# Performance work log

Hardware: AMD Instinct MI355X
Metric: run time of the kernel (lower is better)

## Reference

```python
import jax, jax.numpy as jnp
import numpy as np

N_NODES = 50000
N_EDGES = 800000
D_IN = 128
D_HID = 128
D_OUT = 128
EPS = 0.1  # GINConv eps


def setup_inputs() -> dict:
    key = jax.random.key(0)
    k = jax.random.split(key, 8)
    scale = 1.0 / np.sqrt(D_IN)
    return {
        "x": jax.random.normal(k[0], (N_NODES, D_IN), dtype=jnp.float32),
        "edge_index": jax.random.randint(k[1], (2, N_EDGES), 0, N_NODES, dtype=jnp.int64),
        "edge_weight": jax.random.uniform(k[2], (N_EDGES,), dtype=jnp.float32),
        "W1a": jax.random.normal(k[3], (D_IN, D_HID), dtype=jnp.float32) * scale,
        "W1b": jax.random.normal(k[4], (D_HID, D_HID), dtype=jnpp.float32) if False else jax.random.normal(k[4], (D_HID, D_HID), dtype=jnp.float32) * scale,
        "W2a": jax.random.normal(k[5], (D_HID, D_HID), dtype=jnp.float32) * scale,
        "W2b": jax.random.normal(k[6], (D_HID, D_OUT), dtype=jnp.float32) * scale,
    }


def _gin_conv(h, src, dst, ew, Wa, Wb, n_nodes):
    # edge-weighted neighbor sum: aggr[i] = sum_{(j->i)} w_ji * h[j]
    msg = ew[:, None] * h[src]                       # [E, d]
    aggr = jax.ops.segment_sum(msg, dst, num_segments=n_nodes)  # [N, d]
    z = (1.0 + EPS) * h + aggr                       # GIN update
    # 2-layer bias-free MLP: lin -> relu -> lin
    return jnp.maximum(z @ Wa, 0.0) @ Wb


def reference(x, edge_index, edge_weight, W1a, W1b, W2a, W2b):
    src, dst = edge_index[0], edge_index[1]
    n = x.shape[0]
    h = _gin_conv(x, src, dst, edge_weight, W1a, W1b, n)
    h = jnp.maximum(h, 0.0)  # relu between convs; dropout is identity in eval
    h = _gin_conv(h, src, dst, edge_weight, W2a, W2b, n)
    return h
```

## Files before the change

### kernel.cpp

```cpp
#include <hip/hip_runtime.h>
#include <hip/hip_fp16.h>

#define D 128
#define N_NODES 50000
#define EPSP1 1.1f

#define NPB 128
#define NBUCK 391
#define CAP 2560
#define P1E 4096
#define TS 136

typedef __attribute__((ext_vector_type(8))) short short8;
typedef __attribute__((ext_vector_type(4))) float f32x4;

__device__ __forceinline__ unsigned short f2bf(float f) {
    unsigned u = __float_as_uint(f);
    u += 0x7FFF + ((u >> 16) & 1);
    return (unsigned short)(u >> 16);
}
__device__ __forceinline__ float bf2f(unsigned short h) {
    return __uint_as_float(((unsigned)h) << 16);
}

__global__ __launch_bounds__(512, 4) void pass1_all(
    const int* __restrict__ src, const int* __restrict__ dst,
    const float* __restrict__ ew, int* __restrict__ gcnt,
    uint2* __restrict__ gstage, int ne, int nb1,
    const float* __restrict__ x, unsigned short* __restrict__ hb,
    int n4, int ncvt,
    const float* __restrict__ W1a, const float* __restrict__ W1b,
    const float* __restrict__ W2a, const float* __restrict__ W2b,
    unsigned short* __restrict__ wp)
{
    __shared__ int bcnt[NBUCK];
    __shared__ int goff[NBUCK];
    int tid = threadIdx.x;
    int bid = blockIdx.x;

    if (bid < nb1) {
        for (int i = tid; i < NBUCK; i += 512) bcnt[i] = 0;
        __syncthreads();
        int e0 = bid * P1E;
        int   rank[8];
        int   buck[8];
        uint2 pay[8];
#pragma unroll
        for (int j = 0; j < 8; ++j) {
            int e = e0 + j * 512 + tid;
            buck[j] = -1;
            if (e < ne) {
                int d_ = dst[e];
                int b  = d_ >> 7;
                int dl = d_ & 127;
                pay[j].x = (unsigned)(src[e] & 0xFFFF) | ((unsigned)dl << 16);
                pay[j].y = (unsigned)__half_as_ushort(__float2half_rn(ew[e]));
                rank[j]  = atomicAdd(&bcnt[b], 1);
                buck[j]  = b;
            }
        }
        __syncthreads();
        for (int i = tid; i < NBUCK; i += 512)
            if (bcnt[i] > 0) goff[i] = atomicAdd(&gcnt[i], bcnt[i]);
        __syncthreads();
#pragma unroll
        for (int j = 0; j < 8; ++j) {
            if (buck[j] >= 0) {
                int pos = goff[buck[j]] + rank[j];
                if (pos < CAP)
                    gstage[(size_t)buck[j] * CAP + pos] = pay[j];
            }
        }
    } else if (bid < nb1 + ncvt) {
        int base = (bid - nb1) * 4096;
#pragma unroll
        for (int it = 0; it < 8; ++it) {
            int i = base + it * 512 + tid;
            if (i < n4) {
                float4 v = ((const float4*)x)[i];
                ushort4 o;
                o.x = f2bf(v.x); o.y = f2bf(v.y); o.z = f2bf(v.z); o.w = f2bf(v.w);
                ((ushort4*)hb)[i] = o;
            }
        }
    } else {
        int e2 = (bid - nb1 - ncvt) * 512 + tid;
        if (e2 < 8192) {
            int mat = e2 >> 11;
            int e   = e2 & 2047;
            const float* W = (mat == 0) ? W1a : (mat == 1) ? W1b : (mat == 2) ? W2a : W2b;
            unsigned short* Wp = wp + (size_t)mat * 16384;
            int col = e & 127;
            int kq  = e >> 7;
            short8 v;
#pragma unroll
            for (int j = 0; j < 8; ++j)
                v[j] = (short)f2bf(W[(size_t)(kq * 8 + j) * 128 + col]);
            ((short8*)Wp)[e] = v;
        }
    }
}

__global__ __launch_bounds__(512) void csr_build(
    const uint2* __restrict__ gstage, const int* __restrict__ gcnt,
    unsigned* __restrict__ epay, int* __restrict__ off)
{
    __shared__ int hist[NPB];
    __shared__ int scn[NPB];
    __shared__ int loc[NPB];
    __shared__ int wtot[2];
    __shared__ int base_s;
    __shared__ unsigned csr[CAP];

    int b = blockIdx.x;
    int t = threadIdx.x;
    int cnt = min(gcnt[b], CAP);

    if (t < NPB) hist[t] = 0;
    __syncthreads();

    uint2 ent[CAP / 512];
#pragma unroll
    for (int it = 0; it < CAP / 512; ++it) {
        int i = it * 512 + t;
        if (i < cnt) {
            ent[it] = gstage[(size_t)b * CAP + i];
            atomicAdd(&hist[(ent[it].x >> 16) & 255], 1);
        }
    }
    __syncthreads();

    int w = t >> 6, l = t & 63;
    if (w < 2) {
        int v = hist[w * 64 + l];
#pragma unroll
        for (int dd = 1; dd < 64; dd <<= 1) {
            int u = __shfl_up(v, dd, 64);
            if (l >= dd) v += u;
        }
        scn[w * 64 + l] = v;
        if (l == 63) wtot[w] = v;
    } else if (w == 2) {
        int v = 0;
        for (int i = l; i < NBUCK; i += 64)
            if (i < b) v += min(gcnt[i], CAP);
#pragma unroll
        for (int dd = 32; dd > 0; dd >>= 1) v += __shfl_down(v, dd, 64);
        if (l == 0) base_s = v;
    }
    __syncthreads();

    if (t < NPB) {
        int pre = (t >= 64) ? wtot[0] : 0;
        int incl = scn[t] + pre;
        int excl = incl - hist[t];
        int node = (b << 7) + t;
        if (node <= N_NODES) off[node] = base_s + excl;
        loc[t] = excl;
    }
    __syncthreads();

#pragma unroll
    for (int it = 0; it < CAP / 512; ++it) {
        int i = it * 512 + t;
        if (i < cnt) {
            int dl = (ent[it].x >> 16) & 255;
            int p = atomicAdd(&loc[dl], 1);
            csr[p] = (ent[it].x & 0xFFFF) | (ent[it].y << 16);
        }
    }
    __syncthreads();

    for (int i = t; i < cnt; i += 512)
        epay[base_s + i] = csr[i];
}

template<int RELU2, int OUT_F32>
__global__ __launch_bounds__(512, 8) void conv_fused(
    const unsigned short* __restrict__ h, const int* __restrict__ off,
    const unsigned* __restrict__ epay,
    const unsigned short* __restrict__ WpA,
    const unsigned short* __restrict__ WpB,
    void* __restrict__ outv, int n)
{
    __shared__ unsigned short t1[32 * TS];
    __shared__ unsigned short t2[32 * TS];
    __shared__ int offs[33];

    int tid  = threadIdx.x;
    int wave = tid >> 6;
    int lane = tid & 63;
    int qtr  = lane >> 4;
    int sub  = lane & 15;
    int nb   = blockIdx.x * 32;

    if (tid < 33) offs[tid] = off[min(nb + tid, n)];
    __syncthreads();

    int row  = wave * 4 + qtr;
    int node = nb + row;
    int beg = offs[row];
    int end = offs[row + 1];

    float acc[8];
#pragma unroll
    for (int c = 0; c < 8; ++c) acc[c] = 0.f;

    int i = beg;
    for (; i + 4 <= end; i += 4) {
        unsigned p0 = epay[i];
        unsigned p1 = epay[i + 1];
        unsigned p2 = epay[i + 2];
        unsigned p3 = epay[i + 3];
        short8 v0 = ((const short8*)(h + (size_t)(p0 & 0xFFFF) * D))[sub];
        short8 v1 = ((const short8*)(h + (size_t)(p1 & 0xFFFF) * D))[sub];
        short8 v2 = ((const short8*)(h + (size_t)(p2 & 0xFFFF) * D))[sub];
        short8 v3 = ((const short8*)(h + (size_t)(p3 & 0xFFFF) * D))[sub];
        float w0 = __half2float(__ushort_as_half((unsigned short)(p0 >> 16)));
        float w1 = __half2float(__ushort_as_half((unsigned short)(p1 >> 16)));
        float w2 = __half2float(__ushort_as_half((unsigned short)(p2 >> 16)));
        float w3 = __half2float(__ushort_as_half((unsigned short)(p3 >> 16)));
#pragma unroll
        for (int c = 0; c < 8; ++c)
            acc[c] += w0 * bf2f((unsigned short)v0[c]) + w1 * bf2f((unsigned short)v1[c])
                    + w2 * bf2f((unsigned short)v2[c]) + w3 * bf2f((unsigned short)v3[c]);
    }
    for (; i < end; ++i) {
        unsigned p0 = epay[i];
        short8 v0 = ((const short8*)(h + (size_t)(p0 & 0xFFFF) * D))[sub];
        float w0 = __half2float(__ushort_as_half((unsigned short)(p0 >> 16)));
#pragma unroll
        for (int c = 0; c < 8; ++c)
            acc[c] += w0 * bf2f((unsigned short)v0[c]);
    }

    {
        const short8 zero8 = {0, 0, 0, 0, 0, 0, 0, 0};
        short8 o;
        if (node < n) {
            short8 xv = ((const short8*)(h + (size_t)node * D))[sub];
#pragma unroll
            for (int c = 0; c < 8; ++c)
                o[c] = (short)f2bf(acc[c] + EPSP1 * bf2f((unsigned short)xv[c]));
        } else {
            o = zero8;
        }
        *(short8*)&t1[row * TS + sub * 8] = o;
    }
    __syncthreads();

    int cf = wave;
    f32x4 acc2[2];
    acc2[0] = (f32x4){0.f, 0.f, 0.f, 0.f};
    acc2[1] = (f32x4){0.f, 0.f, 0.f, 0.f};

#pragma unroll
    for (int kk = 0; kk < 4; ++kk) {
        short8 a0 = *(const short8*)&t1[(sub)      * TS + kk * 32 + qtr * 8];
        short8 a1 = *(const short8*)&t1[(16 + sub) * TS + kk * 32 + qtr * 8];
        short8 b  = *(const short8*)(WpA + ((size_t)(kk * 4 + qtr) * 128 + cf * 16 + sub) * 8);
        acc2[0] = __builtin_amdgcn_mfma_f32_16x16x32_bf16(a0, b, acc2[0], 0, 0, 0);
        acc2[1] = __builtin_amdgcn_mfma_f32_16x16x32_bf16(a1, b, acc2[1], 0, 0, 0);
    }

#pragma unroll
    for (int s = 0; s < 2; ++s)
#pragma unroll
        for (int reg = 0; reg < 4; ++reg) {
            int r = s * 16 + qtr * 4 + reg;
            t2[r * TS + cf * 16 + sub] = f2bf(fmaxf(acc2[s][reg], 0.f));
        }
    __syncthreads();

    acc2[0] = (f32x4){0.f, 0.f, 0.f, 0.f};
    acc2[1] = (f32x4){0.f, 0.f, 0.f, 0.f};

#pragma unroll
    for (int kk = 0; kk < 4; ++kk) {
        short8 a0 = *(const short8*)&t2[(sub)      * TS + kk * 32 + qtr * 8];
        short8 a1 = *(const short8*)&t2[(16 + sub) * TS + kk * 32 + qtr * 8];
        short8 b  = *(const short8*)(WpB + ((size_t)(kk * 4 + qtr) * 128 + cf * 16 + sub) * 8);
        acc2[0] = __builtin_amdgcn_mfma_f32_16x16x32_bf16(a0, b, acc2[0], 0, 0, 0);
        acc2[1] = __builtin_amdgcn_mfma_f32_16x16x32_bf16(a1, b, acc2[1], 0, 0, 0);
    }

#pragma unroll
    for (int s = 0; s < 2; ++s)
#pragma unroll
        for (int reg = 0; reg < 4; ++reg) {
            int r = nb + s * 16 + qtr * 4 + reg;
            if (r < n) {
                float v = acc2[s][reg];
                if (RELU2) v = fmaxf(v, 0.f);
                int col = cf * 16 + sub;
                if (OUT_F32)
                    ((float*)outv)[(size_t)r * D + col] = v;
                else
                    ((unsigned short*)outv)[(size_t)r * D + col] = f2bf(v);
            }
        }
}

extern "C" void kernel_launch(void* const* d_in, const int* in_sizes, int n_in,
                              void* d_out, int out_size, void* d_ws, size_t ws_size,
                              hipStream_t stream) {
    const float* x   = (const float*)d_in[0];
    const int*   ei  = (const int*)d_in[1];
    const float* ew  = (const float*)d_in[2];
    const float* W1a = (const float*)d_in[3];
    const float* W1b = (const float*)d_in[4];
    const float* W2a = (const float*)d_in[5];
    const float* W2b = (const float*)d_in[6];
    float* out = (float*)d_out;

    int n_edges = in_sizes[2];
    const int* src = ei;
    const int* dst = ei + n_edges;

    size_t node_elems = (size_t)N_NODES * D;
    unsigned short* hb = (unsigned short*)d_ws;
    unsigned short* zb = hb + node_elems;
    unsigned short* wp = zb + node_elems;
    unsigned* epay = (unsigned*)(wp + 4 * 16384);
    uint2*  gstage = (uint2*)(epay + n_edges);
    int*    gcnt   = (int*)(gstage + (size_t)NBUCK * CAP);
    int*    off    = gcnt + NBUCK;

    int nb1   = (n_edges + P1E - 1) / P1E;
    int n4    = (int)(node_elems / 4);
    int ncvt  = (n4 + 4095) / 4096;
    int npack = 16;
    int cgrid = (N_NODES + 31) / 32;

    hipMemsetAsync(gcnt, 0, NBUCK * sizeof(int), stream);

    pass1_all<<<nb1 + ncvt + npack, 512, 0, stream>>>(
        src, dst, ew, gcnt, gstage, n_edges, nb1,
        x, hb, n4, ncvt, W1a, W1b, W2a, W2b, wp);

    csr_build<<<NBUCK, 512, 0, stream>>>(gstage, gcnt, epay, off);

    unsigned short* wp0 = wp;
    unsigned short* wp1 = wp + 16384;
    unsigned short* wp2 = wp + 2 * 16384;
    unsigned short* wp3 = wp + 3 * 16384;

    conv_fused<1, 0><<<cgrid, 512, 0, stream>>>(hb, off, epay, wp0, wp1, zb, N_NODES);

    conv_fused<0, 1><<<cgrid, 512, 0, stream>>>(zb, off, epay, wp2, wp3, out, N_NODES);
}
```

Measured before the change: 177.9 us.

## Merge all stages into one persistent kernel with software grid barriers

Replaces the four separate kernel launches (bucketing, CSR build, two GIN convolutions) with one persistent kernel of 512 blocks. The blocks loop over work units per stage and separate stages with an atomic-counter grid barrier, and shared memory is overlaid through a union. This removes the launch gaps and tail drain between kernels. In exchange, the conv stages lose occupancy (launch bounds of 4 waves instead of 8, and a fixed 512-block grid), and correctness depends on all 512 blocks being co-resident.

```diff
diff --git a/kernel.cpp b/kernel.cpp
--- a/kernel.cpp
+++ b/kernel.cpp
@@ -10,6 +10,7 @@
 #define CAP 2560
 #define P1E 4096
 #define TS 136
+#define PGRID 512
 
 typedef __attribute__((ext_vector_type(8))) short short8;
 typedef __attribute__((ext_vector_type(4))) float f32x4;
@@ -23,25 +24,48 @@
     return __uint_as_float(((unsigned)h) << 16);
 }
 
-__global__ __launch_bounds__(512, 4) void pass1_all(
+__device__ __forceinline__ void gsync(unsigned* bar) {
+    __syncthreads();
+    if (threadIdx.x == 0) {
+        __threadfence();
+        unsigned old = atomicAdd(bar, 1u);
+        unsigned tgt = (old / PGRID + 1u) * PGRID;
+        while (__hip_atomic_load(bar, __ATOMIC_RELAXED,
+                                 __HIP_MEMORY_SCOPE_AGENT) < tgt)
+            __builtin_amdgcn_s_sleep(2);
+        __threadfence();
+    }
+    __syncthreads();
+}
+
+struct SmemP1 { int bcnt[NBUCK]; int goff[NBUCK]; };
+struct SmemCsr {
+    int hist[NPB]; int scn[NPB]; int loc[NPB];
+    int wtot[2]; int base_s;
+    unsigned csr[CAP];
+};
+struct SmemConv {
+    unsigned short t1[32 * TS];
+    unsigned short t2[32 * TS];
+    int offs[33];
+};
+union SmemAll { SmemP1 p1; SmemCsr c; SmemConv v; };
+
+__device__ __forceinline__ void p1_unit(
+    int u, int nb1, int ncvt, SmemAll& sm,
     const int* __restrict__ src, const int* __restrict__ dst,
     const float* __restrict__ ew, int* __restrict__ gcnt,
-    uint2* __restrict__ gstage, int ne, int nb1,
-    const float* __restrict__ x, unsigned short* __restrict__ hb,
-    int n4, int ncvt,
+    uint2* __restrict__ gstage, int ne,
+    const float* __restrict__ x, unsigned short* __restrict__ hb, int n4,
     const float* __restrict__ W1a, const float* __restrict__ W1b,
     const float* __restrict__ W2a, const float* __restrict__ W2b,
     unsigned short* __restrict__ wp)
 {
-    __shared__ int bcnt[NBUCK];
-    __shared__ int goff[NBUCK];
     int tid = threadIdx.x;
-    int bid = blockIdx.x;
-
-    if (bid < nb1) {
-        for (int i = tid; i < NBUCK; i += 512) bcnt[i] = 0;
+    if (u < nb1) {
+        for (int i = tid; i < NBUCK; i += 512) sm.p1.bcnt[i] = 0;
         __syncthreads();
-        int e0 = bid * P1E;
+        int e0 = u * P1E;
         int   rank[8];
         int   buck[8];
         uint2 pay[8];
@@ -55,24 +79,25 @@
                 int dl = d_ & 127;
                 pay[j].x = (unsigned)(src[e] & 0xFFFF) | ((unsigned)dl << 16);
                 pay[j].y = (unsigned)__half_as_ushort(__float2half_rn(ew[e]));
-                rank[j]  = atomicAdd(&bcnt[b], 1);
+                rank[j]  = atomicAdd(&sm.p1.bcnt[b], 1);
                 buck[j]  = b;
             }
         }
         __syncthreads();
         for (int i = tid; i < NBUCK; i += 512)
-            if (bcnt[i] > 0) goff[i] = atomicAdd(&gcnt[i], bcnt[i]);
+            if (sm.p1.bcnt[i] > 0) sm.p1.goff[i] = atomicAdd(&gcnt[i], sm.p1.bcnt[i]);
         __syncthreads();
 #pragma unroll
         for (int j = 0; j < 8; ++j) {
             if (buck[j] >= 0) {
-                int pos = goff[buck[j]] + rank[j];
+                int pos = sm.p1.goff[buck[j]] + rank[j];
                 if (pos < CAP)
                     gstage[(size_t)buck[j] * CAP + pos] = pay[j];
             }
         }
-    } else if (bid < nb1 + ncvt) {
-        int base = (bid - nb1) * 4096;
+        __syncthreads();
+    } else if (u < nb1 + ncvt) {
+        int base = (u - nb1) * 4096;
 #pragma unroll
         for (int it = 0; it < 8; ++it) {
             int i = base + it * 512 + tid;
@@ -84,7 +109,7 @@
             }
         }
     } else {
-        int e2 = (bid - nb1 - ncvt) * 512 + tid;
+        int e2 = (u - nb1 - ncvt) * 512 + tid;
         if (e2 < 8192) {
             int mat = e2 >> 11;
             int e   = e2 & 2047;
@@ -101,22 +126,15 @@
     }
 }
 
-__global__ __launch_bounds__(512) void csr_build(
+__device__ __forceinline__ void csr_unit(
+    int b, SmemAll& sm,
     const uint2* __restrict__ gstage, const int* __restrict__ gcnt,
     unsigned* __restrict__ epay, int* __restrict__ off)
 {
-    __shared__ int hist[NPB];
-    __shared__ int scn[NPB];
-    __shared__ int loc[NPB];
-    __shared__ int wtot[2];
-    __shared__ int base_s;
-    __shared__ unsigned csr[CAP];
-
-    int b = blockIdx.x;
     int t = threadIdx.x;
     int cnt = min(gcnt[b], CAP);
 
-    if (t < NPB) hist[t] = 0;
+    if (t < NPB) sm.c.hist[t] = 0;
     __syncthreads();
 
     uint2 ent[CAP / 512];
@@ -125,38 +143,38 @@
         int i = it * 512 + t;
         if (i < cnt) {
             ent[it] = gstage[(size_t)b * CAP + i];
-            atomicAdd(&hist[(ent[it].x >> 16) & 255], 1);
+            atomicAdd(&sm.c.hist[(ent[it].x >> 16) & 255], 1);
         }
     }
     __syncthreads();
 
     int w = t >> 6, l = t & 63;
     if (w < 2) {
-        int v = hist[w * 64 + l];
+        int v = sm.c.hist[w * 64 + l];
 #pragma unroll
         for (int dd = 1; dd < 64; dd <<= 1) {
             int u = __shfl_up(v, dd, 64);
             if (l >= dd) v += u;
         }
-        scn[w * 64 + l] = v;
-        if (l == 63) wtot[w] = v;
+        sm.c.scn[w * 64 + l] = v;
+        if (l == 63) sm.c.wtot[w] = v;
     } else if (w == 2) {
         int v = 0;
         for (int i = l; i < NBUCK; i += 64)
             if (i < b) v += min(gcnt[i], CAP);
 #pragma unroll
         for (int dd = 32; dd > 0; dd >>= 1) v += __shfl_down(v, dd, 64);
-        if (l == 0) base_s = v;
+        if (l == 0) sm.c.base_s = v;
     }
     __syncthreads();
 
     if (t < NPB) {
-        int pre = (t >= 64) ? wtot[0] : 0;
-        int incl = scn[t] + pre;
-        int excl = incl - hist[t];
+        int pre = (t >= 64) ? sm.c.wtot[0] : 0;
+        int incl = sm.c.scn[t] + pre;
+        int excl = incl - sm.c.hist[t];
         int node = (b << 7) + t;
-        if (node <= N_NODES) off[node] = base_s + excl;
-        loc[t] = excl;
+        if (node <= N_NODES) off[node] = sm.c.base_s + excl;
+        sm.c.loc[t] = excl;
     }
     __syncthreads();
 
@@ -165,42 +183,41 @@
         int i = it * 512 + t;
         if (i < cnt) {
             int dl = (ent[it].x >> 16) & 255;
-            int p = atomicAdd(&loc[dl], 1);
-            csr[p] = (ent[it].x & 0xFFFF) | (ent[it].y << 16);
-        }
-    }
-    __syncthreads();
-
+            int p = atomicAdd(&sm.c.loc[dl], 1);
+            sm.c.csr[p] = (ent[it].x & 0xFFFF) | (ent[it].y << 16);
+        }
+    }
+    __syncthreads();
+
+    int base_s = sm.c.base_s;
     for (int i = t; i < cnt; i += 512)
-        epay[base_s + i] = csr[i];
+        epay[base_s + i] = sm.c.csr[i];
+    __syncthreads();
 }
 
 template<int RELU2, int OUT_F32>
-__global__ __launch_bounds__(512, 8) void conv_fused(
+__device__ __forceinline__ void conv_unit(
+    int u, SmemAll& sm,
     const unsigned short* __restrict__ h, const int* __restrict__ off,
     const unsigned* __restrict__ epay,
     const unsigned short* __restrict__ WpA,
     const unsigned short* __restrict__ WpB,
     void* __restrict__ outv, int n)
 {
-    __shared__ unsigned short t1[32 * TS];
-    __shared__ unsigned short t2[32 * TS];
-    __shared__ int offs[33];
-
     int tid  = threadIdx.x;
     int wave = tid >> 6;
     int lane = tid & 63;
     int qtr  = lane >> 4;
     int sub  = lane & 15;
-    int nb   = blockIdx.x * 32;
-
-    if (tid < 33) offs[tid] = off[min(nb + tid, n)];
+    int nb   = u * 32;
+
+    if (tid < 33) sm.v.offs[tid] = off[min(nb + tid, n)];
     __syncthreads();
 
     int row  = wave * 4 + qtr;
     int node = nb + row;
-    int beg = offs[row];
-    int end = offs[row + 1];
+    int beg = sm.v.offs[row];
+    int end = sm.v.offs[row + 1];
 
     float acc[8];
 #pragma unroll
@@ -245,7 +262,7 @@
         } else {
             o = zero8;
         }
-        *(short8*)&t1[row * TS + sub * 8] = o;
+        *(short8*)&sm.v.t1[row * TS + sub * 8] = o;
     }
     __syncthreads();
 
@@ -256,8 +273,8 @@
 
 #pragma unroll
     for (int kk = 0; kk < 4; ++kk) {
-        short8 a0 = *(const short8*)&t1[(sub)      * TS + kk * 32 + qtr * 8];
-        short8 a1 = *(const short8*)&t1[(16 + sub) * TS + kk * 32 + qtr * 8];
+        short8 a0 = *(const short8*)&sm.v.t1[(sub)      * TS + kk * 32 + qtr * 8];
+        short8 a1 = *(const short8*)&sm.v.t1[(16 + sub) * TS + kk * 32 + qtr * 8];
         short8 b  = *(const short8*)(WpA + ((size_t)(kk * 4 + qtr) * 128 + cf * 16 + sub) * 8);
         acc2[0] = __builtin_amdgcn_mfma_f32_16x16x32_bf16(a0, b, acc2[0], 0, 0, 0);
         acc2[1] = __builtin_amdgcn_mfma_f32_16x16x32_bf16(a1, b, acc2[1], 0, 0, 0);
@@ -268,7 +285,7 @@
 #pragma unroll
         for (int reg = 0; reg < 4; ++reg) {
             int r = s * 16 + qtr * 4 + reg;
-            t2[r * TS + cf * 16 + sub] = f2bf(fmaxf(acc2[s][reg], 0.f));
+            sm.v.t2[r * TS + cf * 16 + sub] = f2bf(fmaxf(acc2[s][reg], 0.f));
         }
     __syncthreads();
 
@@ -277,8 +294,8 @@
 
 #pragma unroll
     for (int kk = 0; kk < 4; ++kk) {
-        short8 a0 = *(const short8*)&t2[(sub)      * TS + kk * 32 + qtr * 8];
-        short8 a1 = *(const short8*)&t2[(16 + sub) * TS + kk * 32 + qtr * 8];
+        short8 a0 = *(const short8*)&sm.v.t2[(sub)      * TS + kk * 32 + qtr * 8];
+        short8 a1 = *(const short8*)&sm.v.t2[(16 + sub) * TS + kk * 32 + qtr * 8];
         short8 b  = *(const short8*)(WpB + ((size_t)(kk * 4 + qtr) * 128 + cf * 16 + sub) * 8);
         acc2[0] = __builtin_amdgcn_mfma_f32_16x16x32_bf16(a0, b, acc2[0], 0, 0, 0);
         acc2[1] = __builtin_amdgcn_mfma_f32_16x16x32_bf16(a1, b, acc2[1], 0, 0, 0);
@@ -299,6 +316,47 @@
                     ((unsigned short*)outv)[(size_t)r * D + col] = f2bf(v);
             }
         }
+    __syncthreads();
+}
+
+__global__ __launch_bounds__(512, 4) void gin_mega(
+    const int* __restrict__ src, const int* __restrict__ dst,
+    const float* __restrict__ ew, int* __restrict__ gcnt,
+    uint2* __restrict__ gstage, int ne, int nb1,
+    const float* __restrict__ x, unsigned short* __restrict__ hb,
+    int n4, int ncvt,
+    const float* __restrict__ W1a, const float* __restrict__ W1b,
+    const float* __restrict__ W2a, const float* __restrict__ W2b,
+    unsigned short* __restrict__ wp,
+    unsigned* __restrict__ epay, int* __restrict__ off,
+    unsigned short* __restrict__ zb, float* __restrict__ out,
+    unsigned* __restrict__ bar)
+{
+    __shared__ SmemAll sm;
+
+    int bid = blockIdx.x;
+    int cgridn = (N_NODES + 31) / 32;
+
+    int p1units = nb1 + ncvt + 16;
+    for (int u = bid; u < p1units; u += PGRID)
+        p1_unit(u, nb1, ncvt, sm, src, dst, ew, gcnt, gstage, ne,
+                x, hb, n4, W1a, W1b, W2a, W2b, wp);
+    gsync(bar);
+
+    for (int u = bid; u < NBUCK; u += PGRID)
+        csr_unit(u, sm, gstage, gcnt, epay, off);
+    gsync(bar);
+
+    const unsigned short* wp0 = wp;
+    const unsigned short* wp1 = wp + 16384;
+    for (int u = bid; u < cgridn; u += PGRID)
+        conv_unit<1, 0>(u, sm, hb, off, epay, wp0, wp1, (void*)zb, N_NODES);
+    gsync(bar);
+
+    const unsigned short* wp2 = wp + 2 * 16384;
+    const unsigned short* wp3 = wp + 3 * 16384;
+    for (int u = bid; u < cgridn; u += PGRID)
+        conv_unit<0, 1>(u, sm, zb, off, epay, wp2, wp3, (void*)out, N_NODES);
 }
 
 extern "C" void kernel_launch(void* const* d_in, const int* in_sizes, int n_in,
@@ -324,28 +382,17 @@
     unsigned* epay = (unsigned*)(wp + 4 * 16384);
     uint2*  gstage = (uint2*)(epay + n_edges);
     int*    gcnt   = (int*)(gstage + (size_t)NBUCK * CAP);
-    int*    off    = gcnt + NBUCK;
+    unsigned* bar  = (unsigned*)(gcnt + NBUCK);
+    int*    off    = (int*)(bar + 1);
 
     int nb1   = (n_edges + P1E - 1) / P1E;
     int n4    = (int)(node_elems / 4);
     int ncvt  = (n4 + 4095) / 4096;
-    int npack = 16;
-    int cgrid = (N_NODES + 31) / 32;
-
-    hipMemsetAsync(gcnt, 0, NBUCK * sizeof(int), stream);
-
-    pass1_all<<<nb1 + ncvt + npack, 512, 0, stream>>>(
+
+    hipMemsetAsync(gcnt, 0, (NBUCK + 1) * sizeof(int), stream);
+
+    gin_mega<<<PGRID, 512, 0, stream>>>(
         src, dst, ew, gcnt, gstage, n_edges, nb1,
-        x, hb, n4, ncvt, W1a, W1b, W2a, W2b, wp);
-
-    csr_build<<<NBUCK, 512, 0, stream>>>(gstage, gcnt, epay, off);
-
-    unsigned short* wp0 = wp;
-    unsigned short* wp1 = wp + 16384;
-    unsigned short* wp2 = wp + 2 * 16384;
-    unsigned short* wp3 = wp + 3 * 16384;
-
-    conv_fused<1, 0><<<cgrid, 512, 0, stream>>>(hb, off, epay, wp0, wp1, zb, N_NODES);
-
-    conv_fused<0, 1><<<cgrid, 512, 0, stream>>>(zb, off, epay, wp2, wp3, out, N_NODES);
-}
+        x, hb, n4, ncvt, W1a, W1b, W2a, W2b, wp,
+        epay, off, zb, out, bar);
+}
```

Result: slower. 371.4 us (+108.8%).
